# Optimization experiments

Measured on AMD Instinct MI355X. Metric: run time of the kernel, lower is better.

The kernel has to match this reference:

```python
import jax, jax.numpy as jnp
import numpy as np

B, N, HID = 4, 1024, 256
NH, DH = 8, 32          # heads, head dim (HID = NH*DH)
BH = 64                 # bias MLP hidden


def setup_inputs() -> dict:
    key = jax.random.key(0)
    ks = jax.random.split(key, 12)
    s = lambda fan_in: 1.0 / np.sqrt(fan_in)
    return {
        "h": jax.random.normal(ks[0], (B, N, HID), jnp.float32),
        "coord": jax.random.uniform(ks[1], (B, N), jnp.float32),
        "mask": jnp.ones((B, N), jnp.int32),
        # qkv / proj linear params (stored [in, out])
        "Wqkv": jax.random.normal(ks[2], (HID, 3 * HID), jnp.float32) * s(HID),
        "bqkv": jnp.zeros((3 * HID,), jnp.float32),
        "Wproj": jax.random.normal(ks[3], (HID, HID), jnp.float32) * s(HID),
        "bproj": jnp.zeros((HID,), jnp.float32),
        # layernorm
        "gamma": jnp.ones((HID,), jnp.float32),
        "beta": jnp.zeros((HID,), jnp.float32),
        # relative-bias MLP: Linear(1->BH), SiLU, Linear(BH->BH), SiLU, Linear(BH->NH)
        "Wb1": jax.random.normal(ks[4], (1, BH), jnp.float32),
        "bb1": jnp.zeros((BH,), jnp.float32),
        "Wb2": jax.random.normal(ks[5], (BH, BH), jnp.float32) * s(BH),
        "bb2": jnp.zeros((BH,), jnp.float32),
        "Wb3": jax.random.normal(ks[6], (BH, NH), jnp.float32) * s(BH),
        "bb3": jnp.zeros((NH,), jnp.float32),
    }


def _layernorm(x, gamma, beta, eps=1e-5):
    mu = jnp.mean(x, axis=-1, keepdims=True)
    var = jnp.mean((x - mu) ** 2, axis=-1, keepdims=True)
    return (x - mu) * jax.lax.rsqrt(var + eps) * gamma + beta


def reference(h, coord, mask, Wqkv, bqkv, Wproj, bproj, gamma, beta,
              Wb1, bb1, Wb2, bb2, Wb3, bb3):
    x = _layernorm(h, gamma, beta)                      # [B,N,HID]
    qkv = x @ Wqkv + bqkv                               # [B,N,3*HID]
    q, k, v = jnp.split(qkv, 3, axis=-1)
    # [B,N,HID] -> [B,NH,N,DH]
    reshape = lambda t: t.reshape(B, N, NH, DH).transpose(0, 2, 1, 3)
    q, k, v = reshape(q), reshape(k), reshape(v)

    attn = jnp.einsum("bhqd,bhkd->bhqk", q, k) / np.sqrt(DH).astype(np.float32)

    # pairwise coordinate differences and learned bias
    dcoord = coord[:, None, :] - coord[:, :, None]      # [B,N,N]
    t = dcoord[..., None]                               # [B,N,N,1]
    t = jax.nn.silu(t @ Wb1 + bb1)                      # [B,N,N,BH]
    t = jax.nn.silu(t @ Wb2 + bb2)                      # [B,N,N,BH]
    bias = (t @ Wb3 + bb3)                              # [B,N,N,NH]
    attn = attn + bias.transpose(0, 3, 1, 2)            # [B,NH,N,N]

    neg_inf = jnp.array(-jnp.inf, attn.dtype)
    attn = jnp.where(mask[:, None, None, :] == 0, neg_inf, attn)
    w = jax.nn.softmax(attn, axis=-1)

    out = jnp.einsum("bhqk,bhkd->bhqd", w, v)           # [B,NH,N,DH]
    out = out.transpose(0, 2, 1, 3).reshape(B, N, HID)
    out = out @ Wproj + bproj
    return h + out
```

## Files before the change

### kernel.cpp

```cpp
#include <hip/hip_runtime.h>
#include <hip/hip_fp16.h>
#include <math.h>

#define BB   4
#define NN   1024
#define HIDD 256
#define NHD  8
#define DHD  32
#define BHD  64
#define TI4  4096
#define TBS  4104
#define LOG2E 1.4426950408889634f

typedef __attribute__((ext_vector_type(8))) short bf16x8;
typedef __attribute__((ext_vector_type(4))) short bf16x4;
typedef __attribute__((ext_vector_type(4))) float f32x4;

__device__ __forceinline__ unsigned short f2bf(float x) {
  union { float f; unsigned u; } c; c.f = x;
  unsigned r = c.u + 0x7FFFu + ((c.u >> 16) & 1u);
  return (unsigned short)(r >> 16);
}
__device__ __forceinline__ float bf2f(unsigned short b) {
  union { unsigned u; float f; } c; c.u = ((unsigned)b) << 16;
  return c.f;
}

__device__ __forceinline__ void pv_mfma(f32x4& acc, bf16x4 a, bf16x4 b) {
#if __has_builtin(__builtin_amdgcn_mfma_f32_16x16x16bf16_1k)
  acc = __builtin_amdgcn_mfma_f32_16x16x16bf16_1k(a, b, acc, 0, 0, 0);
#else
  asm volatile("s_nop 1\n\t"
               "v_mfma_f32_16x16x16_bf16 %0, %1, %2, %0\n\t"
               "s_nop 7\n\t"
               "s_nop 3"
               : "+v"(acc) : "v"(a), "v"(b));
#endif
}

__global__ __launch_bounds__(256) void prep_kernel(
    const float* __restrict__ Wb1, const float* __restrict__ bb1,
    const float* __restrict__ Wb2, const float* __restrict__ bb2,
    const float* __restrict__ Wb3, const float* __restrict__ bb3,
    const float* __restrict__ Wqkv, const float* __restrict__ Wproj,
    unsigned short* __restrict__ tblb, unsigned short* __restrict__ wtq,
    unsigned short* __restrict__ wtp)
{
  __shared__ float h1a[4][64], h2a[4][64];
  __shared__ float t[16][17];
  int bid = blockIdx.x, tid = threadIdx.x;
  if (bid < 1025) {
    int g = tid >> 6, j = tid & 63;
    int pt = bid * 4 + g;
    float tt = -1.0f + (float)pt * (2.0f / (float)TI4);
    float z0 = fmaf(tt, Wb1[j], bb1[j]);
    h1a[g][j] = z0 / (1.0f + __expf(-z0));
    __syncthreads();
    float a0 = bb2[j];
    #pragma unroll 16
    for (int i = 0; i < BHD; ++i) a0 = fmaf(h1a[g][i], Wb2[i*BHD + j], a0);
    h2a[g][j] = a0 / (1.0f + __expf(-a0));
    __syncthreads();
    if (j < NHD && pt <= TI4) {
      float o0 = bb3[j];
      #pragma unroll 16
      for (int i = 0; i < BHD; ++i) o0 = fmaf(h2a[g][i], Wb3[i*NHD + j], o0);
      tblb[j*TBS + pt] = f2bf(o0 * LOG2E);
    }
  } else {
    const float* W; unsigned short* Wt; int n0, k0, ncols;
    if (bid < 1793) {
      int rb = bid - 1025;
      n0 = (rb % 48) * 16; k0 = (rb / 48) * 16; ncols = 768;
      W = Wqkv; Wt = wtq;
    } else {
      int rc = bid - 1793;
      n0 = (rc & 15) * 16; k0 = (rc >> 4) * 16; ncols = 256;
      W = Wproj; Wt = wtp;
    }
    int sx = tid & 15, sy = tid >> 4;
    t[sy][sx] = W[(size_t)(k0 + sy) * ncols + n0 + sx];
    __syncthreads();
    Wt[(size_t)(n0 + sy) * 256 + k0 + sx] = f2bf(t[sx][sy]);
  }
}

__global__ __launch_bounds__(256) void ln_qkv_mm_kernel(
    const float* __restrict__ h, const float* __restrict__ gamma,
    const float* __restrict__ beta, const unsigned short* __restrict__ Wt,
    const float* __restrict__ bqkv,
    unsigned short* __restrict__ qws, unsigned short* __restrict__ kws,
    unsigned short* __restrict__ vtws)
{
  __shared__ unsigned short xs[16][260];
  int tid = threadIdx.x;
  int m0 = blockIdx.x * 16, n0 = blockIdx.y * 128;

  {
    int r = tid >> 4, q = tid & 15;
    const float* hrow = h + (size_t)(m0 + r)*HIDD + q*16;
    float4 xv[4];
    float sum = 0.f, sq = 0.f;
    #pragma unroll
    for (int j = 0; j < 4; ++j) {
      xv[j] = *(const float4*)&hrow[j*4];
      sum += xv[j].x + xv[j].y + xv[j].z + xv[j].w;
      sq  += xv[j].x*xv[j].x + xv[j].y*xv[j].y + xv[j].z*xv[j].z + xv[j].w*xv[j].w;
    }
    sum += __shfl_xor(sum, 1); sq += __shfl_xor(sq, 1);
    sum += __shfl_xor(sum, 2); sq += __shfl_xor(sq, 2);
    sum += __shfl_xor(sum, 4); sq += __shfl_xor(sq, 4);
    sum += __shfl_xor(sum, 8); sq += __shfl_xor(sq, 8);
    float mu  = sum * (1.0f/HIDD);
    float var = sq  * (1.0f/HIDD) - mu*mu;
    float rs  = rsqrtf(var + 1e-5f);
    #pragma unroll
    for (int j2 = 0; j2 < 2; ++j2) {
      union { bf16x8 v; unsigned short u[8]; } o;
      #pragma unroll
      for (int e = 0; e < 2; ++e) {
        float4 x4 = xv[j2*2 + e];
        int col = q*16 + j2*8 + e*4;
        float4 gv = *(const float4*)&gamma[col];
        float4 bv = *(const float4*)&beta[col];
        o.u[e*4+0] = f2bf(fmaf((x4.x - mu)*rs, gv.x, bv.x));
        o.u[e*4+1] = f2bf(fmaf((x4.y - mu)*rs, gv.y, bv.y));
        o.u[e*4+2] = f2bf(fmaf((x4.z - mu)*rs, gv.z, bv.z));
        o.u[e*4+3] = f2bf(fmaf((x4.w - mu)*rs, gv.w, bv.w));
      }
      *(bf16x8*)&xs[r][q*16 + j2*8] = o.v;
    }
  }
  __syncthreads();

  int lane = tid & 63, w = tid >> 6;
  int lo = lane & 15, hi = lane >> 4;
  int cw = w * 32;
  f32x4 acc[2];
  acc[0] = (f32x4){0.f,0.f,0.f,0.f};
  acc[1] = (f32x4){0.f,0.f,0.f,0.f};

  #pragma unroll
  for (int ks = 0; ks < 8; ++ks) {
    bf16x8 af = *(const bf16x8*)&xs[lo][ks*32 + hi*8];
    #pragma unroll
    for (int nt = 0; nt < 2; ++nt) {
      bf16x8 bf = *(const bf16x8*)&Wt[(size_t)(n0 + cw + nt*16 + lo)*256 + ks*32 + hi*8];
      acc[nt] = __builtin_amdgcn_mfma_f32_16x16x32_bf16(af, bf, acc[nt], 0, 0, 0);
    }
  }

  int b = m0 >> 10;
  if (n0 < 512) {
    unsigned short* dst = (n0 < 256) ? qws : kws;
    int nbase = (m0 & 1023) + hi*4;
    #pragma unroll
    for (int nt = 0; nt < 2; ++nt) {
      int c = n0 + cw + nt*16 + lo;
      int cr = c & 255;
      int head = cr >> 5, d = cr & 31;
      float bq = bqkv[c];
      size_t bh = (size_t)(b*NHD + head);
      #pragma unroll
      for (int r = 0; r < 4; ++r)
        dst[(bh*NN + nbase + r)*DHD + d] = f2bf(acc[nt][r] + bq);
    }
  } else {
    __syncthreads();
    unsigned short (*vt)[20] = (unsigned short(*)[20])&xs[0][0];
    #pragma unroll
    for (int nt = 0; nt < 2; ++nt) {
      int cr = cw + nt*16 + lo;
      float bq = bqkv[n0 + cr];
      union { unsigned short u[4]; unsigned wd[2]; } pk;
      #pragma unroll
      for (int r = 0; r < 4; ++r) pk.u[r] = f2bf(acc[nt][r] + bq);
      int col = hi*4;
      *(unsigned*)&vt[cr][col]     = pk.wd[0];
      *(unsigned*)&vt[cr][col + 2] = pk.wd[1];
    }
    __syncthreads();
    int nn0 = m0 & 1023;
    int row = tid >> 1, ch = tid & 1;
    int cr256 = (n0 - 512) + row;
    int head = cr256 >> 5, d = cr256 & 31;
    *(bf16x8*)&vtws[((size_t)(b*NHD + head)*DHD + d)*NN + nn0 + ch*8] =
        *(const bf16x8*)&vt[row][ch*8];
  }
}

__global__ __launch_bounds__(256, 4) void attn_kernel(
    const unsigned short* __restrict__ Q, const unsigned short* __restrict__ K,
    const unsigned short* __restrict__ Vt, const float* __restrict__ coord,
    const int* __restrict__ mask, const unsigned short* __restrict__ tblb,
    unsigned short* __restrict__ pO, float2* __restrict__ pML)
{
  __shared__ unsigned short tableL[TBS];
  __shared__ unsigned short Klds[2][64][40];
  __shared__ unsigned short Vtlds[2][32][72];

  int tid = threadIdx.x, lane = tid & 63, w = tid >> 6;
  int bh = blockIdx.y, half = blockIdx.z;
  int b = bh >> 3, head = bh & 7;
  int qbase = blockIdx.x * 64 + w * 16;
  int lo = lane & 15, hi = lane >> 4;

  {
    const uint4* src = (const uint4*)(tblb + head*TBS);
    uint4* dst = (uint4*)tableL;
    for (int i = tid; i < TBS/8; i += 256) dst[i] = src[i];
  }

  bf16x8 qf = *(const bf16x8*)&Q[((size_t)bh*NN + qbase + lo)*DHD + hi*8];
  float qoff2 = fmaf(coord[b*NN + qbase + lo], -(float)TI4*0.5f, (float)TI4*0.5f);

  float m = -1e30f, l = 0.f;
  f32x4 oacc[2];
  oacc[0] = (f32x4){0.f,0.f,0.f,0.f};
  oacc[1] = (f32x4){0.f,0.f,0.f,0.f};
  const float scale2 = 0.17677669529663689f * LOG2E;

  int kt0 = half * (NN/2);
  int sr = tid >> 2, ss = tid & 3;
  int vr = tid >> 3, vs = tid & 7;
  {
    *(bf16x8*)&Klds[0][sr][ss*8] =
        *(const bf16x8*)&K[((size_t)bh*NN + kt0 + sr)*DHD + ss*8];
    *(bf16x8*)&Vtlds[0][vr][vs*8] =
        *(const bf16x8*)&Vt[((size_t)bh*DHD + vr)*NN + kt0 + vs*8];
  }
  __syncthreads();

  for (int t = 0; t < 8; ++t) {
    int kt = kt0 + t*64;
    int cur = t & 1;
    bf16x8 kn, vn;
    if (t < 7) {
      kn = *(const bf16x8*)&K[((size_t)bh*NN + kt + 64 + sr)*DHD + ss*8];
      vn = *(const bf16x8*)&Vt[((size_t)bh*DHD + vr)*NN + kt + 64 + vs*8];
    }
    float ck[4][4]; int mk[4][4];
    #pragma unroll
    for (int nt = 0; nt < 4; ++nt) {
      float4 c4 = *(const float4*)&coord[b*NN + kt + nt*16 + hi*4];
      int4   m4 = *(const int4*)  &mask [b*NN + kt + nt*16 + hi*4];
      ck[nt][0] = c4.x; ck[nt][1] = c4.y; ck[nt][2] = c4.z; ck[nt][3] = c4.w;
      mk[nt][0] = m4.x; mk[nt][1] = m4.y; mk[nt][2] = m4.z; mk[nt][3] = m4.w;
    }

    f32x4 z = {0.f,0.f,0.f,0.f};
    f32x4 sacc[4];
    #pragma unroll
    for (int nt = 0; nt < 4; ++nt) {
      bf16x8 kf = *(const bf16x8*)&Klds[cur][nt*16 + lo][hi*8];
      sacc[nt] = __builtin_amdgcn_mfma_f32_16x16x32_bf16(kf, qf, z, 0, 0, 0);
    }

    float sv[4][4];
    #pragma unroll
    for (int nt = 0; nt < 4; ++nt) {
      #pragma unroll
      for (int r = 0; r < 4; ++r) {
        float u = fmaf(ck[nt][r], (float)TI4*0.5f, qoff2);
        int i0 = (int)(u + 0.5f);
        float bias = bf2f(tableL[i0]);
        float s = fmaf(sacc[nt][r], scale2, bias);
        sv[nt][r] = mk[nt][r] ? s : -1e31f;
      }
    }

    float pm = sv[0][0];
    #pragma unroll
    for (int nt = 0; nt < 4; ++nt)
      #pragma unroll
      for (int r = 0; r < 4; ++r) pm = fmaxf(pm, sv[nt][r]);
    pm = fmaxf(pm, __shfl_xor(pm, 16));
    pm = fmaxf(pm, __shfl_xor(pm, 32));
    float mn = fmaxf(m, pm);
    if (mn > m) {
      float sf = __builtin_amdgcn_exp2f(m - mn);
      l *= sf;
      #pragma unroll
      for (int n2 = 0; n2 < 2; ++n2)
        #pragma unroll
        for (int r = 0; r < 4; ++r) oacc[n2][r] *= sf;
      m = mn;
    }

    bf16x4 pfrag[4];
    #pragma unroll
    for (int nt = 0; nt < 4; ++nt) {
      float p0 = __builtin_amdgcn_exp2f(sv[nt][0] - m);
      float p1 = __builtin_amdgcn_exp2f(sv[nt][1] - m);
      float p2 = __builtin_amdgcn_exp2f(sv[nt][2] - m);
      float p3 = __builtin_amdgcn_exp2f(sv[nt][3] - m);
      l += (p0 + p1) + (p2 + p3);
      union { bf16x4 v; unsigned short u[4]; } pk;
      pk.u[0] = f2bf(p0); pk.u[1] = f2bf(p1);
      pk.u[2] = f2bf(p2); pk.u[3] = f2bf(p3);
      pfrag[nt] = pk.v;
    }

    #pragma unroll
    for (int nt = 0; nt < 4; ++nt) {
      #pragma unroll
      for (int n2 = 0; n2 < 2; ++n2) {
        bf16x4 vf = *(const bf16x4*)&Vtlds[cur][n2*16 + lo][nt*16 + hi*4];
        pv_mfma(oacc[n2], vf, pfrag[nt]);
      }
    }

    if (t < 7) {
      *(bf16x8*)&Klds[cur^1][sr][ss*8] = kn;
      *(bf16x8*)&Vtlds[cur^1][vr][vs*8] = vn;
    }
    __syncthreads();
  }

  l += __shfl_xor(l, 16);
  l += __shfl_xor(l, 32);
  size_t base = ((size_t)(half*BB*NHD + bh)*NN + qbase + lo);
  #pragma unroll
  for (int n2 = 0; n2 < 2; ++n2) {
    union { bf16x4 v; unsigned short u[4]; } ov;
    ov.u[0] = f2bf(oacc[n2][0]); ov.u[1] = f2bf(oacc[n2][1]);
    ov.u[2] = f2bf(oacc[n2][2]); ov.u[3] = f2bf(oacc[n2][3]);
    *(bf16x4*)&pO[base*DHD + n2*16 + hi*4] = ov.v;
  }
  if (hi == 0) pML[base] = make_float2(m, l);
}

__global__ __launch_bounds__(256) void combine_kernel(
    const unsigned short* __restrict__ pO, const float2* __restrict__ pML,
    unsigned short* __restrict__ aob)
{
  int idx = blockIdx.x * 256 + threadIdx.x;
  int rg = idx >> 2, d8 = (idx & 3) << 3;
  int bh = rg >> 10, n = rg & 1023;
  int b = bh >> 3, head = bh & 7;
  float2 ml0 = pML[rg];
  float2 ml1 = pML[(size_t)(BB*NHD)*NN + rg];
  float mm = fmaxf(ml0.x, ml1.x);
  float e0 = __builtin_amdgcn_exp2f(ml0.x - mm);
  float e1 = __builtin_amdgcn_exp2f(ml1.x - mm);
  float inv = 1.0f / fmaf(ml0.y, e0, ml1.y * e1);
  e0 *= inv; e1 *= inv;
  union { bf16x8 v; unsigned short u[8]; } a, c, o;
  a.v = *(const bf16x8*)&pO[(size_t)rg*DHD + d8];
  c.v = *(const bf16x8*)&pO[((size_t)(BB*NHD)*NN + rg)*DHD + d8];
  #pragma unroll
  for (int e = 0; e < 8; ++e)
    o.u[e] = f2bf(fmaf(bf2f(a.u[e]), e0, bf2f(c.u[e]) * e1));
  *(bf16x8*)&aob[((size_t)(b*NN + n))*HIDD + head*DHD + d8] = o.v;
}

__global__ __launch_bounds__(256) void proj_mm_kernel(
    const unsigned short* __restrict__ AO, const unsigned short* __restrict__ Wpt,
    const float* __restrict__ bp, const float* __restrict__ h,
    float* __restrict__ out)
{
  int tid = threadIdx.x, lane = tid & 63, w = tid >> 6;
  int lo = lane & 15, hi = lane >> 4;
  int m0 = blockIdx.x * 32 + (w & 1) * 16;
  int n0 = blockIdx.y * 32 + (w >> 1) * 16;
  f32x4 acc = (f32x4){0.f,0.f,0.f,0.f};

  #pragma unroll
  for (int ks = 0; ks < 8; ++ks) {
    bf16x8 af = *(const bf16x8*)&AO[(size_t)(m0 + lo)*256 + ks*32 + hi*8];
    bf16x8 bf = *(const bf16x8*)&Wpt[(size_t)(n0 + lo)*256 + ks*32 + hi*8];
    acc = __builtin_amdgcn_mfma_f32_16x16x32_bf16(af, bf, acc, 0, 0, 0);
  }

  int c = n0 + lo;
  float bpv = bp[c];
  #pragma unroll
  for (int r = 0; r < 4; ++r) {
    size_t o = (size_t)(m0 + hi*4 + r)*HIDD + c;
    out[o] = h[o] + acc[r] + bpv;
  }
}

extern "C" void kernel_launch(void* const* d_in, const int* in_sizes, int n_in,
                              void* d_out, int out_size, void* d_ws, size_t ws_size,
                              hipStream_t stream)
{
  const float* h     = (const float*)d_in[0];
  const float* coord = (const float*)d_in[1];
  const int*   mask  = (const int*)  d_in[2];
  const float* Wqkv  = (const float*)d_in[3];
  const float* bqkv  = (const float*)d_in[4];
  const float* Wproj = (const float*)d_in[5];
  const float* bproj = (const float*)d_in[6];
  const float* gamma = (const float*)d_in[7];
  const float* beta  = (const float*)d_in[8];
  const float* Wb1   = (const float*)d_in[9];
  const float* bb1   = (const float*)d_in[10];
  const float* Wb2   = (const float*)d_in[11];
  const float* bb2   = (const float*)d_in[12];
  const float* Wb3   = (const float*)d_in[13];
  const float* bb3   = (const float*)d_in[14];
  float* out = (float*)d_out;

  unsigned short* tblb = (unsigned short*)d_ws;
  float2* pML = (float2*)(tblb + NHD*TBS);
  unsigned short* wtq  = (unsigned short*)(pML + (size_t)2*BB*NHD*NN);
  unsigned short* wtp  = wtq + 768*256;
  unsigned short* qws  = wtp + 256*256;
  unsigned short* kws  = qws + (size_t)BB*NHD*NN*DHD;
  unsigned short* vtws = kws + (size_t)BB*NHD*NN*DHD;
  unsigned short* pO   = vtws + (size_t)BB*NHD*NN*DHD;
  unsigned short* aob  = pO + (size_t)2*BB*NHD*NN*DHD;

  prep_kernel<<<dim3(2049), dim3(256), 0, stream>>>(
      Wb1, bb1, Wb2, bb2, Wb3, bb3, Wqkv, Wproj, tblb, wtq, wtp);
  ln_qkv_mm_kernel<<<dim3(BB*NN/16, 6), dim3(256), 0, stream>>>(
      h, gamma, beta, wtq, bqkv, qws, kws, vtws);
  attn_kernel<<<dim3(NN/64, BB*NHD, 2), dim3(256), 0, stream>>>(
      qws, kws, vtws, coord, mask, tblb, pO, pML);
  combine_kernel<<<dim3(512), dim3(256), 0, stream>>>(pO, pML, aob);
  proj_mm_kernel<<<dim3(BB*NN/32, HIDD/32), dim3(256), 0, stream>>>(
      aob, wtp, bproj, h, out);
}
```

Measured before the change: 65.24 us.

## Split attention keys four ways and halve the bias lookup table

Attention over keys is now split into four partitions instead of two, and the combine kernel merges four partial softmax results. This gives more blocks in flight and a shorter serial loop per block. The bias lookup table is halved from 4096 to 2048 entries, which shrinks prep work and LDS per block and allows a higher occupancy hint (6). In exchange, partial-output traffic doubles, the combine does more work, and the coarser table lowers bias interpolation accuracy.

```diff
diff --git a/kernel.cpp b/kernel.cpp
--- a/kernel.cpp
+++ b/kernel.cpp
@@ -8,8 +8,9 @@
 #define NHD  8
 #define DHD  32
 #define BHD  64
-#define TI4  4096
-#define TBS  4104
+#define TI2  2048
+#define TBS2 2056
+#define NSPL 4
 #define LOG2E 1.4426950408889634f
 
 typedef __attribute__((ext_vector_type(8))) short bf16x8;
@@ -49,10 +50,10 @@
   __shared__ float h1a[4][64], h2a[4][64];
   __shared__ float t[16][17];
   int bid = blockIdx.x, tid = threadIdx.x;
-  if (bid < 1025) {
+  if (bid < 513) {
     int g = tid >> 6, j = tid & 63;
     int pt = bid * 4 + g;
-    float tt = -1.0f + (float)pt * (2.0f / (float)TI4);
+    float tt = -1.0f + (float)pt * (2.0f / (float)TI2);
     float z0 = fmaf(tt, Wb1[j], bb1[j]);
     h1a[g][j] = z0 / (1.0f + __expf(-z0));
     __syncthreads();
@@ -61,20 +62,20 @@
     for (int i = 0; i < BHD; ++i) a0 = fmaf(h1a[g][i], Wb2[i*BHD + j], a0);
     h2a[g][j] = a0 / (1.0f + __expf(-a0));
     __syncthreads();
-    if (j < NHD && pt <= TI4) {
+    if (j < NHD && pt <= TI2) {
       float o0 = bb3[j];
       #pragma unroll 16
       for (int i = 0; i < BHD; ++i) o0 = fmaf(h2a[g][i], Wb3[i*NHD + j], o0);
-      tblb[j*TBS + pt] = f2bf(o0 * LOG2E);
+      tblb[j*TBS2 + pt] = f2bf(o0 * LOG2E);
     }
   } else {
     const float* W; unsigned short* Wt; int n0, k0, ncols;
-    if (bid < 1793) {
-      int rb = bid - 1025;
+    if (bid < 1281) {
+      int rb = bid - 513;
       n0 = (rb % 48) * 16; k0 = (rb / 48) * 16; ncols = 768;
       W = Wqkv; Wt = wtq;
     } else {
-      int rc = bid - 1793;
+      int rc = bid - 1281;
       n0 = (rc & 15) * 16; k0 = (rc >> 4) * 16; ncols = 256;
       W = Wproj; Wt = wtp;
     }
@@ -189,30 +190,30 @@
   }
 }
 
-__global__ __launch_bounds__(256, 4) void attn_kernel(
+__global__ __launch_bounds__(256, 6) void attn_kernel(
     const unsigned short* __restrict__ Q, const unsigned short* __restrict__ K,
     const unsigned short* __restrict__ Vt, const float* __restrict__ coord,
     const int* __restrict__ mask, const unsigned short* __restrict__ tblb,
     unsigned short* __restrict__ pO, float2* __restrict__ pML)
 {
-  __shared__ unsigned short tableL[TBS];
+  __shared__ unsigned short tableL[TBS2];
   __shared__ unsigned short Klds[2][64][40];
   __shared__ unsigned short Vtlds[2][32][72];
 
   int tid = threadIdx.x, lane = tid & 63, w = tid >> 6;
-  int bh = blockIdx.y, half = blockIdx.z;
+  int bh = blockIdx.y, quarter = blockIdx.z;
   int b = bh >> 3, head = bh & 7;
   int qbase = blockIdx.x * 64 + w * 16;
   int lo = lane & 15, hi = lane >> 4;
 
   {
-    const uint4* src = (const uint4*)(tblb + head*TBS);
+    const uint4* src = (const uint4*)(tblb + head*TBS2);
     uint4* dst = (uint4*)tableL;
-    for (int i = tid; i < TBS/8; i += 256) dst[i] = src[i];
+    for (int i = tid; i < TBS2/8; i += 256) dst[i] = src[i];
   }
 
   bf16x8 qf = *(const bf16x8*)&Q[((size_t)bh*NN + qbase + lo)*DHD + hi*8];
-  float qoff2 = fmaf(coord[b*NN + qbase + lo], -(float)TI4*0.5f, (float)TI4*0.5f);
+  float qoff2 = fmaf(coord[b*NN + qbase + lo], -(float)TI2*0.5f, (float)TI2*0.5f);
 
   float m = -1e30f, l = 0.f;
   f32x4 oacc[2];
@@ -220,7 +221,7 @@
   oacc[1] = (f32x4){0.f,0.f,0.f,0.f};
   const float scale2 = 0.17677669529663689f * LOG2E;
 
-  int kt0 = half * (NN/2);
+  int kt0 = quarter * (NN/NSPL);
   int sr = tid >> 2, ss = tid & 3;
   int vr = tid >> 3, vs = tid & 7;
   {
@@ -231,11 +232,11 @@
   }
   __syncthreads();
 
-  for (int t = 0; t < 8; ++t) {
+  for (int t = 0; t < NN/NSPL/64; ++t) {
     int kt = kt0 + t*64;
     int cur = t & 1;
     bf16x8 kn, vn;
-    if (t < 7) {
+    if (t < NN/NSPL/64 - 1) {
       kn = *(const bf16x8*)&K[((size_t)bh*NN + kt + 64 + sr)*DHD + ss*8];
       vn = *(const bf16x8*)&Vt[((size_t)bh*DHD + vr)*NN + kt + 64 + vs*8];
     }
@@ -261,7 +262,7 @@
     for (int nt = 0; nt < 4; ++nt) {
       #pragma unroll
       for (int r = 0; r < 4; ++r) {
-        float u = fmaf(ck[nt][r], (float)TI4*0.5f, qoff2);
+        float u = fmaf(ck[nt][r], (float)TI2*0.5f, qoff2);
         int i0 = (int)(u + 0.5f);
         float bias = bf2f(tableL[i0]);
         float s = fmaf(sacc[nt][r], scale2, bias);
@@ -310,7 +311,7 @@
       }
     }
 
-    if (t < 7) {
+    if (t < NN/NSPL/64 - 1) {
       *(bf16x8*)&Klds[cur^1][sr][ss*8] = kn;
       *(bf16x8*)&Vtlds[cur^1][vr][vs*8] = vn;
     }
@@ -319,7 +320,7 @@
 
   l += __shfl_xor(l, 16);
   l += __shfl_xor(l, 32);
-  size_t base = ((size_t)(half*BB*NHD + bh)*NN + qbase + lo);
+  size_t base = ((size_t)(quarter*BB*NHD + bh)*NN + qbase + lo);
   #pragma unroll
   for (int n2 = 0; n2 < 2; ++n2) {
     union { bf16x4 v; unsigned short u[4]; } ov;
@@ -338,19 +339,31 @@
   int rg = idx >> 2, d8 = (idx & 3) << 3;
   int bh = rg >> 10, n = rg & 1023;
   int b = bh >> 3, head = bh & 7;
-  float2 ml0 = pML[rg];
-  float2 ml1 = pML[(size_t)(BB*NHD)*NN + rg];
-  float mm = fmaxf(ml0.x, ml1.x);
-  float e0 = __builtin_amdgcn_exp2f(ml0.x - mm);
-  float e1 = __builtin_amdgcn_exp2f(ml1.x - mm);
-  float inv = 1.0f / fmaf(ml0.y, e0, ml1.y * e1);
-  e0 *= inv; e1 *= inv;
-  union { bf16x8 v; unsigned short u[8]; } a, c, o;
-  a.v = *(const bf16x8*)&pO[(size_t)rg*DHD + d8];
-  c.v = *(const bf16x8*)&pO[((size_t)(BB*NHD)*NN + rg)*DHD + d8];
-  #pragma unroll
-  for (int e = 0; e < 8; ++e)
-    o.u[e] = f2bf(fmaf(bf2f(a.u[e]), e0, bf2f(c.u[e]) * e1));
+  const size_t stride = (size_t)(BB*NHD)*NN;
+  float2 ml[NSPL];
+  #pragma unroll
+  for (int j = 0; j < NSPL; ++j) ml[j] = pML[j*stride + rg];
+  float mm = fmaxf(fmaxf(ml[0].x, ml[1].x), fmaxf(ml[2].x, ml[3].x));
+  float e[NSPL];
+  float den = 0.f;
+  #pragma unroll
+  for (int j = 0; j < NSPL; ++j) {
+    e[j] = __builtin_amdgcn_exp2f(ml[j].x - mm);
+    den = fmaf(ml[j].y, e[j], den);
+  }
+  float inv = 1.0f / den;
+  float acc[8] = {0.f,0.f,0.f,0.f,0.f,0.f,0.f,0.f};
+  #pragma unroll
+  for (int j = 0; j < NSPL; ++j) {
+    union { bf16x8 v; unsigned short u[8]; } a;
+    a.v = *(const bf16x8*)&pO[(j*stride + rg)*DHD + d8];
+    float wj = e[j] * inv;
+    #pragma unroll
+    for (int q = 0; q < 8; ++q) acc[q] = fmaf(bf2f(a.u[q]), wj, acc[q]);
+  }
+  union { bf16x8 v; unsigned short u[8]; } o;
+  #pragma unroll
+  for (int q = 0; q < 8; ++q) o.u[q] = f2bf(acc[q]);
   *(bf16x8*)&aob[((size_t)(b*NN + n))*HIDD + head*DHD + d8] = o.v;
 }
 
@@ -403,20 +416,20 @@
   float* out = (float*)d_out;
 
   unsigned short* tblb = (unsigned short*)d_ws;
-  float2* pML = (float2*)(tblb + NHD*TBS);
-  unsigned short* wtq  = (unsigned short*)(pML + (size_t)2*BB*NHD*NN);
+  float2* pML = (float2*)(tblb + NHD*TBS2);
+  unsigned short* wtq  = (unsigned short*)(pML + (size_t)NSPL*BB*NHD*NN);
   unsigned short* wtp  = wtq + 768*256;
   unsigned short* qws  = wtp + 256*256;
   unsigned short* kws  = qws + (size_t)BB*NHD*NN*DHD;
   unsigned short* vtws = kws + (size_t)BB*NHD*NN*DHD;
   unsigned short* pO   = vtws + (size_t)BB*NHD*NN*DHD;
-  unsigned short* aob  = pO + (size_t)2*BB*NHD*NN*DHD;
-
-  prep_kernel<<<dim3(2049), dim3(256), 0, stream>>>(
+  unsigned short* aob  = pO + (size_t)NSPL*BB*NHD*NN*DHD;
+
+  prep_kernel<<<dim3(1537), dim3(256), 0, stream>>>(
       Wb1, bb1, Wb2, bb2, Wb3, bb3, Wqkv, Wproj, tblb, wtq, wtp);
   ln_qkv_mm_kernel<<<dim3(BB*NN/16, 6), dim3(256), 0, stream>>>(
       h, gamma, beta, wtq, bqkv, qws, kws, vtws);
-  attn_kernel<<<dim3(NN/64, BB*NHD, 2), dim3(256), 0, stream>>>(
+  attn_kernel<<<dim3(NN/64, BB*NHD, NSPL), dim3(256), 0, stream>>>(
       qws, kws, vtws, coord, mask, tblb, pO, pML);
   combine_kernel<<<dim3(512), dim3(256), 0, stream>>>(pO, pML, aob);
   proj_mm_kernel<<<dim3(BB*NN/32, HIDD/32), dim3(256), 0, stream>>>(
```

Result: no change. 66.37 us (+1.7%).
